# Optimization experiments

Hardware: AMD Instinct MI355X
Metric: run time of the kernel (lower is better)

Reference implementation:

```python
import jax, jax.numpy as jnp
import numpy as np

CONV_ORDER = 3


def _aggr_norm(L, x):
    # neighborhood_size = row sums of operator; 1/ns with non-finite -> 0
    inv = 1.0 / jnp.sum(L, axis=1)
    inv = jnp.where(jnp.isfinite(inv), inv, 0.0)
    x = inv[:, None] * x
    return jnp.where(jnp.isfinite(x), x, 0.0)


def _chebyshev_conv(L, x, conv_order=CONV_ORDER, aggr_norm=True):
    # Returns [N, C, conv_order]: X[...,k] = norm(L @ X[...,k-1]), X[...,-1 base] = x
    def step(carry, _):
        y = L @ carry
        if aggr_norm:
            y = _aggr_norm(L, y)
        return y, y
    _, X = jax.lax.scan(step, x, None, length=conv_order)  # [K, N, C]
    return jnp.moveaxis(X, 0, -1)  # [N, C, K]


def setup_inputs() -> dict:
    key = jax.random.key(0)
    ks = jax.random.split(key, 13)
    N0, N1, N2, C = 4096, 8192, 4096, 16
    w_scale = 1.414 * np.sqrt(2.0 / (C + C))  # xavier_normal-like
    return {
        "x_0": jax.random.normal(ks[0], (N0, C), jnp.float32),
        "x_1": jax.random.normal(ks[1], (N1, C), jnp.float32),
        "x_2": jax.random.normal(ks[2], (N2, C), jnp.float32),
        "laplacian_0": jax.random.normal(ks[3], (N0, N0), jnp.float32),
        "laplacian_down_1": jax.random.normal(ks[4], (N1, N1), jnp.float32),
        "laplacian_up_1": jax.random.normal(ks[5], (N1, N1), jnp.float32),
        "laplacian_down_2": jax.random.normal(ks[6], (N2, N2), jnp.float32),
        "laplacian_up_2": jax.random.normal(ks[7], (N2, N2), jnp.float32),
        "b1": jax.random.normal(ks[8], (N0, N1), jnp.float32),
        "b2": jax.random.normal(ks[9], (N1, N2), jnp.float32),
        "weight_0": w_scale * jax.random.normal(ks[10], (C, C, 2 + 2 * CONV_ORDER), jnp.float32),
        "weight_1": w_scale * jax.random.normal(ks[11], (C, C, 6 * CONV_ORDER + 3), jnp.float32),
        "weight_2": w_scale * jax.random.normal(ks[12], (C, C, 4 * CONV_ORDER + 2), jnp.float32),
    }


def reference(x_0, x_1, x_2, laplacian_0, laplacian_down_1, laplacian_up_1,
              laplacian_down_2, laplacian_up_2, b1, b2,
              weight_0, weight_1, weight_2):
    # Node-space convolution (the torch forward returns only y_0; the edge/face
    # branches are dead code w.r.t. the returned value and are omitted).
    x_0_lap = _chebyshev_conv(laplacian_0, x_0)                 # [N0, C, K]
    x_0_to_0 = jnp.concatenate([x_0[:, :, None], x_0_lap], axis=2)
    x_1_to_0_upper = b1 @ x_1                                   # [N0, C]
    x_1_to_0_lap = _chebyshev_conv(laplacian_0, x_1_to_0_upper)
    x_1_to_0 = jnp.concatenate([x_1_to_0_upper[:, :, None], x_1_to_0_lap], axis=2)
    x_0_all = jnp.concatenate([x_0_to_0, x_1_to_0], axis=2)     # [N0, C, 2+2K]
    y_0 = jnp.einsum('nik,iok->no', x_0_all, weight_0)
    return y_0
```

## Files before the change

### kernel.cpp

```cpp
#include <hip/hip_runtime.h>
#include <hip/hip_bf16.h>
#include <math.h>

#define N0 4096
#define NM1 8192

#define OFF_XL1 0
#define OFF_XL2 65536
#define OFF_UL1 131072
#define OFF_UL2 196608
#define OFF_INV 262144
#define OFF_PB  266240
#define OFF_PX  528384
#define OFF_PU  1052672
#define OFF_PRS 1576960

template<int NV>
__device__ __forceinline__ void red_scatter(float* v, const int d, const int lane) {
  const bool up = (lane & d) != 0;
  #pragma unroll
  for (int i = 0; i < NV; ++i) {
    float send = up ? v[i] : v[i + NV];
    float recv = __shfl_xor(send, d);
    float keep = up ? v[i + NV] : v[i];
    v[i] = keep + recv;
  }
}

__global__ __launch_bounds__(256)
void b1_matmul_kernel(const float* __restrict__ A,
                      const float* __restrict__ X,
                      float* __restrict__ pP)
{
  __shared__ float4 Bs[2048];
  const int tid  = threadIdx.x;
  const int wv   = tid >> 6;
  const int lane = tid & 63;
  const int q    = lane >> 5;
  const int ml   = lane & 31;
  const int s    = blockIdx.x & 3;
  const int rg   = blockIdx.x >> 2;
  const int row0 = rg * 16 + wv * 4;

  float acc[32];
  #pragma unroll
  for (int i = 0; i < 32; ++i) acc[i] = 0.0f;
  const int j0 = q * 2;
  const int jj = tid & 3;
  const int mt = tid >> 2;

  for (int ch = 0; ch < 4; ++ch) {
    const int mb = s * 2048 + ch * 512;
    __syncthreads();
    #pragma unroll
    for (int k = 0; k < 8; ++k) {
      const int m = mt + 64 * k;
      Bs[(m * 4 + jj) ^ ((m >> 2) & 7)] =
          *(const float4*)(X + (size_t)(mb + m) * 16 + jj * 4);
    }
    __syncthreads();
    #pragma unroll
    for (int it = 0; it < 4; ++it) {
      const int mloc = it * 128 + ml * 4;
      float a[4][4];
      #pragma unroll
      for (int r = 0; r < 4; ++r) {
        const float4 t4 = *(const float4*)(A + (size_t)(row0 + r) * NM1 + mb + mloc);
        a[r][0] = t4.x; a[r][1] = t4.y; a[r][2] = t4.z; a[r][3] = t4.w;
      }
      #pragma unroll
      for (int v = 0; v < 4; ++v) {
        const int mm = mloc + v;
        const int h = (mm >> 2) & 7;
        const float4 b0  = Bs[(mm * 4 + j0) ^ h];
        const float4 b1v = Bs[(mm * 4 + j0 + 1) ^ h];
        #pragma unroll
        for (int r = 0; r < 4; ++r) {
          const float av = a[r][v];
          acc[r*8+0] += av * b0.x;   acc[r*8+1] += av * b0.y;
          acc[r*8+2] += av * b0.z;   acc[r*8+3] += av * b0.w;
          acc[r*8+4] += av * b1v.x;  acc[r*8+5] += av * b1v.y;
          acc[r*8+6] += av * b1v.z;  acc[r*8+7] += av * b1v.w;
        }
      }
    }
  }

  red_scatter<16>(acc, 1, lane);
  red_scatter<8>(acc, 2, lane);
  red_scatter<4>(acc, 4, lane);
  red_scatter<2>(acc, 8, lane);
  red_scatter<1>(acc, 16, lane);

  const int r = 2 * (ml & 1) + ((ml >> 1) & 1);
  const int c = 4 * ((ml >> 2) & 1) + 2 * ((ml >> 3) & 1) + ((ml >> 4) & 1);
  pP[(size_t)(s * N0 + row0 + r) * 16 + q * 8 + c] = acc[0];
}

template<bool RS, bool SUMU>
__global__ __launch_bounds__(256)
void cheb_kernel(const float* __restrict__ A,
                 const float* __restrict__ cx,
                 const float* __restrict__ cu,
                 float* __restrict__ pX,
                 float* __restrict__ pU,
                 float* __restrict__ pRS)
{
  __shared__ float4 Bs[2048];
  const int tid  = threadIdx.x;
  const int wv   = tid >> 6;
  const int lane = tid & 63;
  const int q    = lane >> 3;
  const int ml   = lane & 7;
  const int s    = blockIdx.x & 7;
  const int rg   = blockIdx.x >> 3;
  const int row0 = rg * 32 + wv * 8;
  const int mbase = s * 512;

  float acc[32];
  #pragma unroll
  for (int i = 0; i < 32; ++i) acc[i] = 0.0f;
  float rs[8] = {};

  const int jj = tid & 7;
  const int mt = tid >> 3;
  const float* sbase = (jj < 4) ? cx : cu;
  const int joff = (jj & 3) * 4;

  #pragma unroll 1
  for (int ch = 0; ch < 2; ++ch) {
    const int mb = mbase + ch * 256;
    __syncthreads();
    #pragma unroll
    for (int k = 0; k < 8; ++k) {
      const int m = mt + 32 * k;
      float4 val;
      if constexpr (SUMU) {
        if (jj >= 4) {
          const float* pb = cu + (size_t)(mb + m) * 16 + joff;
          const float4 t0 = *(const float4*)(pb);
          const float4 t1 = *(const float4*)(pb + 65536);
          const float4 t2 = *(const float4*)(pb + 131072);
          const float4 t3 = *(const float4*)(pb + 196608);
          val = make_float4(t0.x + t1.x + t2.x + t3.x,
                            t0.y + t1.y + t2.y + t3.y,
                            t0.z + t1.z + t2.z + t3.z,
                            t0.w + t1.w + t2.w + t3.w);
        } else {
          val = *(const float4*)(cx + (size_t)(mb + m) * 16 + joff);
        }
      } else {
        val = *(const float4*)(sbase + (size_t)(mb + m) * 16 + joff);
      }
      Bs[(m * 8 + jj) ^ ((m >> 2) & 7)] = val;
    }
    __syncthreads();
    #pragma unroll 2
    for (int it = 0; it < 8; ++it) {
      const int mloc = it * 32 + ml * 4;
      float a_[8][4];
      #pragma unroll
      for (int r = 0; r < 8; ++r) {
        const float4 t4 = *(const float4*)(A + (size_t)(row0 + r) * N0 + mb + mloc);
        a_[r][0] = t4.x; a_[r][1] = t4.y; a_[r][2] = t4.z; a_[r][3] = t4.w;
      }
      #pragma unroll
      for (int v = 0; v < 4; ++v) {
        const int mm = mloc + v;
        const float4 b0 = Bs[(mm * 8 + q) ^ ((mm >> 2) & 7)];
        #pragma unroll
        for (int r = 0; r < 8; ++r) {
          const float av = a_[r][v];
          acc[r*4+0] += av * b0.x;  acc[r*4+1] += av * b0.y;
          acc[r*4+2] += av * b0.z;  acc[r*4+3] += av * b0.w;
          if constexpr (RS) rs[r] += av;
        }
      }
    }
  }

  red_scatter<16>(acc, 1, lane);
  red_scatter<8>(acc, 2, lane);
  red_scatter<4>(acc, 4, lane);

  const int r = 4 * (ml & 1) + 2 * ((ml >> 1) & 1) + ((ml >> 2) & 1);
  float* base = (q >> 2) ? pU : pX;
  *(float4*)(base + (size_t)(s * 65536) + (row0 + r) * 16 + (q & 3) * 4) =
      make_float4(acc[0], acc[1], acc[2], acc[3]);

  if constexpr (RS) {
    red_scatter<4>(rs, 1, lane);
    red_scatter<2>(rs, 2, lane);
    red_scatter<1>(rs, 4, lane);
    if (q == 0) pRS[s * N0 + row0 + r] = rs[0];
  }
}

__global__ void norm1_kernel(const float* __restrict__ pX,
                             const float* __restrict__ pU,
                             const float* __restrict__ pRS,
                             float* __restrict__ inv,
                             float* __restrict__ ox,
                             float* __restrict__ ou) {
  const int idx = blockIdx.x * 256 + threadIdx.x;
  const int row = idx >> 4;
  float rsv = 0.0f;
  #pragma unroll
  for (int s2 = 0; s2 < 8; ++s2) rsv += pRS[s2 * N0 + row];
  float iv = 1.0f / rsv;
  if (!isfinite(iv)) iv = 0.0f;
  if ((idx & 15) == 0) inv[row] = iv;
  float xv = 0.0f, uv = 0.0f;
  #pragma unroll
  for (int s2 = 0; s2 < 8; ++s2) { xv += pX[s2*65536 + idx]; uv += pU[s2*65536 + idx]; }
  xv *= iv; uv *= iv;
  ox[idx] = isfinite(xv) ? xv : 0.0f;
  ou[idx] = isfinite(uv) ? uv : 0.0f;
}

__global__ void norm23_kernel(const float* __restrict__ pX,
                              const float* __restrict__ pU,
                              const float* __restrict__ inv,
                              float* __restrict__ ox,
                              float* __restrict__ ou) {
  const int idx = blockIdx.x * 256 + threadIdx.x;
  const float iv = inv[idx >> 4];
  float xv = 0.0f, uv = 0.0f;
  #pragma unroll
  for (int s2 = 0; s2 < 8; ++s2) { xv += pX[s2*65536 + idx]; uv += pU[s2*65536 + idx]; }
  xv *= iv; uv *= iv;
  ox[idx] = isfinite(xv) ? xv : 0.0f;
  ou[idx] = isfinite(uv) ? uv : 0.0f;
}

__global__ void einsum_kernel(const float* __restrict__ x0,
                              const float* __restrict__ xl1,
                              const float* __restrict__ xl2,
                              const float* __restrict__ pB,
                              const float* __restrict__ ul1,
                              const float* __restrict__ ul2,
                              const float* __restrict__ pX,
                              const float* __restrict__ pU,
                              const float* __restrict__ inv,
                              const float* __restrict__ W,
                              float* __restrict__ y) {
  __shared__ float Wl[2048];
  __shared__ float xs[16 * 128];
  const int t = threadIdx.x;
  const int row0 = blockIdx.x * 16;
  #pragma unroll
  for (int k = 0; k < 8; ++k) Wl[t + 256 * k] = W[t + 256 * k];
  const int r = t >> 4;
  const int i = t & 15;
  const int g = (row0 + r) * 16 + i;
  const float iv = inv[row0 + r];
  float x3 = 0.0f, u3 = 0.0f;
  #pragma unroll
  for (int s2 = 0; s2 < 8; ++s2) { x3 += pX[s2*65536 + g]; u3 += pU[s2*65536 + g]; }
  x3 *= iv; u3 *= iv;
  if (!isfinite(x3)) x3 = 0.0f;
  if (!isfinite(u3)) u3 = 0.0f;
  const float uval = pB[g] + pB[65536 + g] + pB[131072 + g] + pB[196608 + g];
  xs[r*128 + 0*16 + i] = x0[g];
  xs[r*128 + 1*16 + i] = xl1[g];
  xs[r*128 + 2*16 + i] = xl2[g];
  xs[r*128 + 3*16 + i] = x3;
  xs[r*128 + 4*16 + i] = uval;
  xs[r*128 + 5*16 + i] = ul1[g];
  xs[r*128 + 6*16 + i] = ul2[g];
  xs[r*128 + 7*16 + i] = u3;
  __syncthreads();
  const int o = t & 15;
  float a = 0.0f;
  #pragma unroll
  for (int ii = 0; ii < 16; ++ii) {
    #pragma unroll
    for (int k = 0; k < 8; ++k)
      a += xs[r*128 + k*16 + ii] * Wl[(ii*16 + o)*8 + k];
  }
  y[(row0 + r) * 16 + o] = a;
}

extern "C" void kernel_launch(void* const* d_in, const int* in_sizes, int n_in,
                              void* d_out, int out_size, void* d_ws, size_t ws_size,
                              hipStream_t stream) {
  (void)in_sizes; (void)n_in; (void)out_size; (void)ws_size;
  const float* x0 = (const float*)d_in[0];
  const float* x1 = (const float*)d_in[1];
  const float* L0 = (const float*)d_in[3];
  const float* B1 = (const float*)d_in[8];
  const float* W0 = (const float*)d_in[10];

  float* ws  = (float*)d_ws;
  float* xl1 = ws + OFF_XL1;
  float* xl2 = ws + OFF_XL2;
  float* ul1 = ws + OFF_UL1;
  float* ul2 = ws + OFF_UL2;
  float* inv = ws + OFF_INV;
  float* pB  = ws + OFF_PB;
  float* pX  = ws + OFF_PX;
  float* pU  = ws + OFF_PU;
  float* pRS = ws + OFF_PRS;

  b1_matmul_kernel<<<1024, 256, 0, stream>>>(B1, x1, pB);

  cheb_kernel<true, true><<<1024, 256, 0, stream>>>(L0, x0, pB, pX, pU, pRS);
  norm1_kernel<<<256, 256, 0, stream>>>(pX, pU, pRS, inv, xl1, ul1);
  cheb_kernel<false, false><<<1024, 256, 0, stream>>>(L0, xl1, ul1, pX, pU, pRS);
  norm23_kernel<<<256, 256, 0, stream>>>(pX, pU, inv, xl2, ul2);
  cheb_kernel<false, false><<<1024, 256, 0, stream>>>(L0, xl2, ul2, pX, pU, pRS);

  einsum_kernel<<<256, 256, 0, stream>>>(x0, xl1, xl2, pB, ul1, ul2,
                                         pX, pU, inv, W0, (float*)d_out);
}
```

Baseline: 134.5 us.

## Fuse all phases into one persistent kernel with hierarchical grid barriers

Replaces the seven separate kernel launches with a single persistent kernel of 512 blocks that runs the b1 matmul, three Chebyshev steps, two normalisations and the einsum as phases separated by a two-level atomic grid barrier. Each block now handles two K-slices per matmul phase instead of one. The goal is to remove launch gaps and tail effects between the small dependent kernels. In exchange it relies on all 512 blocks being co-resident (launch_bounds 256,2), which is not guaranteed, adds barrier spin overhead, and uses half the number of blocks in each matmul phase.

```diff
diff --git a/kernel.cpp b/kernel.cpp
--- a/kernel.cpp
+++ b/kernel.cpp
@@ -14,6 +14,28 @@
 #define OFF_PX  528384
 #define OFF_PU  1052672
 #define OFF_PRS 1576960
+#define OFF_BAR 1609728
+#define REL_OFF 1632
+#define BAR_INTS 1648
+
+__device__ __forceinline__ void grid_barrier(int* bar, int bi) {
+  __syncthreads();
+  if (threadIdx.x == 0) {
+    const int gid = blockIdx.x >> 5;
+    int* grp  = bar + (bi * 17 + gid) * 16;
+    int* root = bar + (bi * 17 + 16) * 16;
+    int* rel  = bar + REL_OFF;
+    if (__hip_atomic_fetch_add(grp, 1, __ATOMIC_ACQ_REL, __HIP_MEMORY_SCOPE_AGENT) == 31) {
+      if (__hip_atomic_fetch_add(root, 1, __ATOMIC_ACQ_REL, __HIP_MEMORY_SCOPE_AGENT) == 15) {
+        __hip_atomic_store(rel, bi + 1, __ATOMIC_RELEASE, __HIP_MEMORY_SCOPE_AGENT);
+      }
+    }
+    while (__hip_atomic_load(rel, __ATOMIC_ACQUIRE, __HIP_MEMORY_SCOPE_AGENT) < bi + 1) {
+      __builtin_amdgcn_s_sleep(2);
+    }
+  }
+  __syncthreads();
+}
 
 template<int NV>
 __device__ __forceinline__ void red_scatter(float* v, const int d, const int lane) {
@@ -27,100 +49,95 @@
   }
 }
 
-__global__ __launch_bounds__(256)
-void b1_matmul_kernel(const float* __restrict__ A,
-                      const float* __restrict__ X,
-                      float* __restrict__ pP)
-{
-  __shared__ float4 Bs[2048];
+__device__ __forceinline__ void b1_phase(const float* __restrict__ A,
+                                         const float* __restrict__ X,
+                                         float* __restrict__ pP,
+                                         float4* Bs) {
   const int tid  = threadIdx.x;
   const int wv   = tid >> 6;
   const int lane = tid & 63;
   const int q    = lane >> 5;
   const int ml   = lane & 31;
-  const int s    = blockIdx.x & 3;
-  const int rg   = blockIdx.x >> 2;
+  const int sb   = blockIdx.x & 1;
+  const int rg   = blockIdx.x >> 1;
   const int row0 = rg * 16 + wv * 4;
-
-  float acc[32];
-  #pragma unroll
-  for (int i = 0; i < 32; ++i) acc[i] = 0.0f;
   const int j0 = q * 2;
   const int jj = tid & 3;
   const int mt = tid >> 2;
 
-  for (int ch = 0; ch < 4; ++ch) {
-    const int mb = s * 2048 + ch * 512;
-    __syncthreads();
+  #pragma unroll 1
+  for (int si = 0; si < 2; ++si) {
+    const int s = sb + 2 * si;
+    float acc[32];
     #pragma unroll
-    for (int k = 0; k < 8; ++k) {
-      const int m = mt + 64 * k;
-      Bs[(m * 4 + jj) ^ ((m >> 2) & 7)] =
-          *(const float4*)(X + (size_t)(mb + m) * 16 + jj * 4);
-    }
-    __syncthreads();
-    #pragma unroll
-    for (int it = 0; it < 4; ++it) {
-      const int mloc = it * 128 + ml * 4;
-      float a[4][4];
+    for (int i = 0; i < 32; ++i) acc[i] = 0.0f;
+
+    #pragma unroll 1
+    for (int ch = 0; ch < 4; ++ch) {
+      const int mb = s * 2048 + ch * 512;
+      __syncthreads();
       #pragma unroll
-      for (int r = 0; r < 4; ++r) {
-        const float4 t4 = *(const float4*)(A + (size_t)(row0 + r) * NM1 + mb + mloc);
-        a[r][0] = t4.x; a[r][1] = t4.y; a[r][2] = t4.z; a[r][3] = t4.w;
-      }
+      for (int k = 0; k < 8; ++k) {
+        const int m = mt + 64 * k;
+        Bs[(m * 4 + jj) ^ ((m >> 2) & 7)] =
+            *(const float4*)(X + (size_t)(mb + m) * 16 + jj * 4);
+      }
+      __syncthreads();
       #pragma unroll
-      for (int v = 0; v < 4; ++v) {
-        const int mm = mloc + v;
-        const int h = (mm >> 2) & 7;
-        const float4 b0  = Bs[(mm * 4 + j0) ^ h];
-        const float4 b1v = Bs[(mm * 4 + j0 + 1) ^ h];
+      for (int it = 0; it < 4; ++it) {
+        const int mloc = it * 128 + ml * 4;
+        float a[4][4];
         #pragma unroll
         for (int r = 0; r < 4; ++r) {
-          const float av = a[r][v];
-          acc[r*8+0] += av * b0.x;   acc[r*8+1] += av * b0.y;
-          acc[r*8+2] += av * b0.z;   acc[r*8+3] += av * b0.w;
-          acc[r*8+4] += av * b1v.x;  acc[r*8+5] += av * b1v.y;
-          acc[r*8+6] += av * b1v.z;  acc[r*8+7] += av * b1v.w;
-        }
-      }
-    }
-  }
-
-  red_scatter<16>(acc, 1, lane);
-  red_scatter<8>(acc, 2, lane);
-  red_scatter<4>(acc, 4, lane);
-  red_scatter<2>(acc, 8, lane);
-  red_scatter<1>(acc, 16, lane);
-
-  const int r = 2 * (ml & 1) + ((ml >> 1) & 1);
-  const int c = 4 * ((ml >> 2) & 1) + 2 * ((ml >> 3) & 1) + ((ml >> 4) & 1);
-  pP[(size_t)(s * N0 + row0 + r) * 16 + q * 8 + c] = acc[0];
+          const float4 t4 = *(const float4*)(A + (size_t)(row0 + r) * NM1 + mb + mloc);
+          a[r][0] = t4.x; a[r][1] = t4.y; a[r][2] = t4.z; a[r][3] = t4.w;
+        }
+        #pragma unroll
+        for (int v = 0; v < 4; ++v) {
+          const int mm = mloc + v;
+          const int h = (mm >> 2) & 7;
+          const float4 b0  = Bs[(mm * 4 + j0) ^ h];
+          const float4 b1v = Bs[(mm * 4 + j0 + 1) ^ h];
+          #pragma unroll
+          for (int r = 0; r < 4; ++r) {
+            const float av = a[r][v];
+            acc[r*8+0] += av * b0.x;   acc[r*8+1] += av * b0.y;
+            acc[r*8+2] += av * b0.z;   acc[r*8+3] += av * b0.w;
+            acc[r*8+4] += av * b1v.x;  acc[r*8+5] += av * b1v.y;
+            acc[r*8+6] += av * b1v.z;  acc[r*8+7] += av * b1v.w;
+          }
+        }
+      }
+    }
+
+    red_scatter<16>(acc, 1, lane);
+    red_scatter<8>(acc, 2, lane);
+    red_scatter<4>(acc, 4, lane);
+    red_scatter<2>(acc, 8, lane);
+    red_scatter<1>(acc, 16, lane);
+
+    const int r = 2 * (ml & 1) + ((ml >> 1) & 1);
+    const int c = 4 * ((ml >> 2) & 1) + 2 * ((ml >> 3) & 1) + ((ml >> 4) & 1);
+    pP[(size_t)(s * N0 + row0 + r) * 16 + q * 8 + c] = acc[0];
+  }
 }
 
 template<bool RS, bool SUMU>
-__global__ __launch_bounds__(256)
-void cheb_kernel(const float* __restrict__ A,
-                 const float* __restrict__ cx,
-                 const float* __restrict__ cu,
-                 float* __restrict__ pX,
-                 float* __restrict__ pU,
-                 float* __restrict__ pRS)
-{
-  __shared__ float4 Bs[2048];
+__device__ __forceinline__ void cheb_phase(const float* __restrict__ A,
+                                           const float* __restrict__ cx,
+                                           const float* __restrict__ cu,
+                                           float* __restrict__ pX,
+                                           float* __restrict__ pU,
+                                           float* __restrict__ pRS,
+                                           float4* Bs) {
   const int tid  = threadIdx.x;
   const int wv   = tid >> 6;
   const int lane = tid & 63;
   const int q    = lane >> 3;
   const int ml   = lane & 7;
-  const int s    = blockIdx.x & 7;
-  const int rg   = blockIdx.x >> 3;
+  const int sb   = blockIdx.x & 3;
+  const int rg   = blockIdx.x >> 2;
   const int row0 = rg * 32 + wv * 8;
-  const int mbase = s * 512;
-
-  float acc[32];
-  #pragma unroll
-  for (int i = 0; i < 32; ++i) acc[i] = 0.0f;
-  float rs[8] = {};
 
   const int jj = tid & 7;
   const int mt = tid >> 3;
@@ -128,88 +145,104 @@
   const int joff = (jj & 3) * 4;
 
   #pragma unroll 1
-  for (int ch = 0; ch < 2; ++ch) {
-    const int mb = mbase + ch * 256;
-    __syncthreads();
+  for (int si = 0; si < 2; ++si) {
+    const int s = sb + 4 * si;
+    const int mbase = s * 512;
+    float acc[32];
     #pragma unroll
-    for (int k = 0; k < 8; ++k) {
-      const int m = mt + 32 * k;
-      float4 val;
-      if constexpr (SUMU) {
-        if (jj >= 4) {
-          const float* pb = cu + (size_t)(mb + m) * 16 + joff;
-          const float4 t0 = *(const float4*)(pb);
-          const float4 t1 = *(const float4*)(pb + 65536);
-          const float4 t2 = *(const float4*)(pb + 131072);
-          const float4 t3 = *(const float4*)(pb + 196608);
-          val = make_float4(t0.x + t1.x + t2.x + t3.x,
-                            t0.y + t1.y + t2.y + t3.y,
-                            t0.z + t1.z + t2.z + t3.z,
-                            t0.w + t1.w + t2.w + t3.w);
+    for (int i = 0; i < 32; ++i) acc[i] = 0.0f;
+    float rs[8] = {};
+
+    #pragma unroll 1
+    for (int ch = 0; ch < 2; ++ch) {
+      const int mb = mbase + ch * 256;
+      __syncthreads();
+      #pragma unroll
+      for (int k = 0; k < 8; ++k) {
+        const int m = mt + 32 * k;
+        float4 val;
+        if constexpr (SUMU) {
+          if (jj >= 4) {
+            const float* pb = cu + (size_t)(mb + m) * 16 + joff;
+            const float4 t0 = *(const float4*)(pb);
+            const float4 t1 = *(const float4*)(pb + 65536);
+            const float4 t2 = *(const float4*)(pb + 131072);
+            const float4 t3 = *(const float4*)(pb + 196608);
+            val = make_float4(t0.x + t1.x + t2.x + t3.x,
+                              t0.y + t1.y + t2.y + t3.y,
+                              t0.z + t1.z + t2.z + t3.z,
+                              t0.w + t1.w + t2.w + t3.w);
+          } else {
+            val = *(const float4*)(cx + (size_t)(mb + m) * 16 + joff);
+          }
         } else {
-          val = *(const float4*)(cx + (size_t)(mb + m) * 16 + joff);
-        }
-      } else {
-        val = *(const float4*)(sbase + (size_t)(mb + m) * 16 + joff);
-      }
-      Bs[(m * 8 + jj) ^ ((m >> 2) & 7)] = val;
-    }
-    __syncthreads();
-    #pragma unroll 2
-    for (int it = 0; it < 8; ++it) {
-      const int mloc = it * 32 + ml * 4;
-      float a_[8][4];
-      #pragma unroll
-      for (int r = 0; r < 8; ++r) {
-        const float4 t4 = *(const float4*)(A + (size_t)(row0 + r) * N0 + mb + mloc);
-        a_[r][0] = t4.x; a_[r][1] = t4.y; a_[r][2] = t4.z; a_[r][3] = t4.w;
-      }
-      #pragma unroll
-      for (int v = 0; v < 4; ++v) {
-        const int mm = mloc + v;
-        const float4 b0 = Bs[(mm * 8 + q) ^ ((mm >> 2) & 7)];
+          val = *(const float4*)(sbase + (size_t)(mb + m) * 16 + joff);
+        }
+        Bs[(m * 8 + jj) ^ ((m >> 2) & 7)] = val;
+      }
+      __syncthreads();
+      #pragma unroll 2
+      for (int it = 0; it < 8; ++it) {
+        const int mloc = it * 32 + ml * 4;
+        float a_[8][4];
         #pragma unroll
         for (int r = 0; r < 8; ++r) {
-          const float av = a_[r][v];
-          acc[r*4+0] += av * b0.x;  acc[r*4+1] += av * b0.y;
-          acc[r*4+2] += av * b0.z;  acc[r*4+3] += av * b0.w;
-          if constexpr (RS) rs[r] += av;
-        }
-      }
-    }
-  }
-
-  red_scatter<16>(acc, 1, lane);
-  red_scatter<8>(acc, 2, lane);
-  red_scatter<4>(acc, 4, lane);
-
-  const int r = 4 * (ml & 1) + 2 * ((ml >> 1) & 1) + ((ml >> 2) & 1);
-  float* base = (q >> 2) ? pU : pX;
-  *(float4*)(base + (size_t)(s * 65536) + (row0 + r) * 16 + (q & 3) * 4) =
-      make_float4(acc[0], acc[1], acc[2], acc[3]);
-
-  if constexpr (RS) {
-    red_scatter<4>(rs, 1, lane);
-    red_scatter<2>(rs, 2, lane);
-    red_scatter<1>(rs, 4, lane);
-    if (q == 0) pRS[s * N0 + row0 + r] = rs[0];
-  }
-}
-
-__global__ void norm1_kernel(const float* __restrict__ pX,
-                             const float* __restrict__ pU,
-                             const float* __restrict__ pRS,
-                             float* __restrict__ inv,
-                             float* __restrict__ ox,
-                             float* __restrict__ ou) {
+          const float4 t4 = *(const float4*)(A + (size_t)(row0 + r) * N0 + mb + mloc);
+          a_[r][0] = t4.x; a_[r][1] = t4.y; a_[r][2] = t4.z; a_[r][3] = t4.w;
+        }
+        #pragma unroll
+        for (int v = 0; v < 4; ++v) {
+          const int mm = mloc + v;
+          const float4 b0 = Bs[(mm * 8 + q) ^ ((mm >> 2) & 7)];
+          #pragma unroll
+          for (int r = 0; r < 8; ++r) {
+            const float av = a_[r][v];
+            acc[r*4+0] += av * b0.x;  acc[r*4+1] += av * b0.y;
+            acc[r*4+2] += av * b0.z;  acc[r*4+3] += av * b0.w;
+            if constexpr (RS) rs[r] += av;
+          }
+        }
+      }
+    }
+
+    red_scatter<16>(acc, 1, lane);
+    red_scatter<8>(acc, 2, lane);
+    red_scatter<4>(acc, 4, lane);
+
+    const int r = 4 * (ml & 1) + 2 * ((ml >> 1) & 1) + ((ml >> 2) & 1);
+    float* base = (q >> 2) ? pU : pX;
+    *(float4*)(base + (size_t)(s * 65536) + (row0 + r) * 16 + (q & 3) * 4) =
+        make_float4(acc[0], acc[1], acc[2], acc[3]);
+
+    if constexpr (RS) {
+      red_scatter<4>(rs, 1, lane);
+      red_scatter<2>(rs, 2, lane);
+      red_scatter<1>(rs, 4, lane);
+      if (q == 0) pRS[s * N0 + row0 + r] = rs[0];
+    }
+  }
+}
+
+template<bool FIRST>
+__device__ __forceinline__ void norm_phase(const float* __restrict__ pX,
+                                           const float* __restrict__ pU,
+                                           const float* __restrict__ pRS,
+                                           float* __restrict__ inv,
+                                           float* __restrict__ ox,
+                                           float* __restrict__ ou) {
   const int idx = blockIdx.x * 256 + threadIdx.x;
   const int row = idx >> 4;
-  float rsv = 0.0f;
-  #pragma unroll
-  for (int s2 = 0; s2 < 8; ++s2) rsv += pRS[s2 * N0 + row];
-  float iv = 1.0f / rsv;
-  if (!isfinite(iv)) iv = 0.0f;
-  if ((idx & 15) == 0) inv[row] = iv;
+  float iv;
+  if constexpr (FIRST) {
+    float rsv = 0.0f;
+    #pragma unroll
+    for (int s2 = 0; s2 < 8; ++s2) rsv += pRS[s2 * N0 + row];
+    iv = 1.0f / rsv;
+    if (!isfinite(iv)) iv = 0.0f;
+    if ((idx & 15) == 0) inv[row] = iv;
+  } else {
+    iv = inv[row];
+  }
   float xv = 0.0f, uv = 0.0f;
   #pragma unroll
   for (int s2 = 0; s2 < 8; ++s2) { xv += pX[s2*65536 + idx]; uv += pU[s2*65536 + idx]; }
@@ -218,34 +251,20 @@
   ou[idx] = isfinite(uv) ? uv : 0.0f;
 }
 
-__global__ void norm23_kernel(const float* __restrict__ pX,
-                              const float* __restrict__ pU,
-                              const float* __restrict__ inv,
-                              float* __restrict__ ox,
-                              float* __restrict__ ou) {
-  const int idx = blockIdx.x * 256 + threadIdx.x;
-  const float iv = inv[idx >> 4];
-  float xv = 0.0f, uv = 0.0f;
-  #pragma unroll
-  for (int s2 = 0; s2 < 8; ++s2) { xv += pX[s2*65536 + idx]; uv += pU[s2*65536 + idx]; }
-  xv *= iv; uv *= iv;
-  ox[idx] = isfinite(xv) ? xv : 0.0f;
-  ou[idx] = isfinite(uv) ? uv : 0.0f;
-}
-
-__global__ void einsum_kernel(const float* __restrict__ x0,
-                              const float* __restrict__ xl1,
-                              const float* __restrict__ xl2,
-                              const float* __restrict__ pB,
-                              const float* __restrict__ ul1,
-                              const float* __restrict__ ul2,
-                              const float* __restrict__ pX,
-                              const float* __restrict__ pU,
-                              const float* __restrict__ inv,
-                              const float* __restrict__ W,
-                              float* __restrict__ y) {
-  __shared__ float Wl[2048];
-  __shared__ float xs[16 * 128];
+__device__ __forceinline__ void einsum_phase(const float* __restrict__ x0,
+                                             const float* __restrict__ xl1,
+                                             const float* __restrict__ xl2,
+                                             const float* __restrict__ pB,
+                                             const float* __restrict__ ul1,
+                                             const float* __restrict__ ul2,
+                                             const float* __restrict__ pX,
+                                             const float* __restrict__ pU,
+                                             const float* __restrict__ inv,
+                                             const float* __restrict__ W,
+                                             float* __restrict__ y,
+                                             float* smem) {
+  float* Wl = smem;
+  float* xs = smem + 2048;
   const int t = threadIdx.x;
   const int row0 = blockIdx.x * 16;
   #pragma unroll
@@ -281,6 +300,42 @@
   y[(row0 + r) * 16 + o] = a;
 }
 
+__global__ void init_bar_kernel(int* bar) {
+  for (int i = threadIdx.x; i < BAR_INTS; i += 256) bar[i] = 0;
+}
+
+__global__ __launch_bounds__(256, 2)
+void mega_kernel(const float* __restrict__ x0, const float* __restrict__ x1,
+                 const float* __restrict__ L0, const float* __restrict__ B1,
+                 const float* __restrict__ W0, float* __restrict__ ws,
+                 int* __restrict__ bar, float* __restrict__ y) {
+  __shared__ float4 Bs[2048];
+  float* xl1 = ws + OFF_XL1;
+  float* xl2 = ws + OFF_XL2;
+  float* ul1 = ws + OFF_UL1;
+  float* ul2 = ws + OFF_UL2;
+  float* inv = ws + OFF_INV;
+  float* pB  = ws + OFF_PB;
+  float* pX  = ws + OFF_PX;
+  float* pU  = ws + OFF_PU;
+  float* pRS = ws + OFF_PRS;
+
+  b1_phase(B1, x1, pB, Bs);
+  grid_barrier(bar, 0);
+  cheb_phase<true, true>(L0, x0, pB, pX, pU, pRS, Bs);
+  grid_barrier(bar, 1);
+  if (blockIdx.x < 256) norm_phase<true>(pX, pU, pRS, inv, xl1, ul1);
+  grid_barrier(bar, 2);
+  cheb_phase<false, false>(L0, xl1, ul1, pX, pU, pRS, Bs);
+  grid_barrier(bar, 3);
+  if (blockIdx.x < 256) norm_phase<false>(pX, pU, pRS, inv, xl2, ul2);
+  grid_barrier(bar, 4);
+  cheb_phase<false, false>(L0, xl2, ul2, pX, pU, pRS, Bs);
+  grid_barrier(bar, 5);
+  if (blockIdx.x < 256)
+    einsum_phase(x0, xl1, xl2, pB, ul1, ul2, pX, pU, inv, W0, y, (float*)Bs);
+}
+
 extern "C" void kernel_launch(void* const* d_in, const int* in_sizes, int n_in,
                               void* d_out, int out_size, void* d_ws, size_t ws_size,
                               hipStream_t stream) {
@@ -291,25 +346,9 @@
   const float* B1 = (const float*)d_in[8];
   const float* W0 = (const float*)d_in[10];
 
-  float* ws  = (float*)d_ws;
-  float* xl1 = ws + OFF_XL1;
-  float* xl2 = ws + OFF_XL2;
-  float* ul1 = ws + OFF_UL1;
-  float* ul2 = ws + OFF_UL2;
-  float* inv = ws + OFF_INV;
-  float* pB  = ws + OFF_PB;
-  float* pX  = ws + OFF_PX;
-  float* pU  = ws + OFF_PU;
-  float* pRS = ws + OFF_PRS;
-
-  b1_matmul_kernel<<<1024, 256, 0, stream>>>(B1, x1, pB);
-
-  cheb_kernel<true, true><<<1024, 256, 0, stream>>>(L0, x0, pB, pX, pU, pRS);
-  norm1_kernel<<<256, 256, 0, stream>>>(pX, pU, pRS, inv, xl1, ul1);
-  cheb_kernel<false, false><<<1024, 256, 0, stream>>>(L0, xl1, ul1, pX, pU, pRS);
-  norm23_kernel<<<256, 256, 0, stream>>>(pX, pU, inv, xl2, ul2);
-  cheb_kernel<false, false><<<1024, 256, 0, stream>>>(L0, xl2, ul2, pX, pU, pRS);
-
-  einsum_kernel<<<256, 256, 0, stream>>>(x0, xl1, xl2, pB, ul1, ul2,
-                                         pX, pU, inv, W0, (float*)d_out);
-}
+  float* ws = (float*)d_ws;
+  int* bar = (int*)(ws + OFF_BAR);
+
+  init_bar_kernel<<<1, 256, 0, stream>>>(bar);
+  mega_kernel<<<512, 256, 0, stream>>>(x0, x1, L0, B1, W0, ws, bar, (float*)d_out);
+}
```

Result: slower. 408.9 us (+203.9%).
